# Kernel optimization log

Hardware: AMD Instinct MI355X
Metric: run time of the kernel (lower is better)

The kernel has to match this reference:

```python
import jax, jax.numpy as jnp
import numpy as np


def setup_inputs() -> dict:
    key = jax.random.key(0)
    k1, k2, k3 = jax.random.split(key, 3)
    B, N = 1024, 4096
    kp3d = jax.random.normal(k1, (B, N, 3), dtype=jnp.float32)
    ref_points = jax.random.uniform(k2, (B, N, 2), dtype=jnp.float32)
    weight = jax.random.uniform(k3, (B, N), dtype=jnp.float32)
    return {"kp3d": kp3d, "ref_points": ref_points, "weight": weight}


def reference(kp3d, ref_points, weight):
    # Projected 2D coords (perspective output already applied upstream).
    x = (kp3d[:, :, 0] + 1.0) * 0.5          # [B, N]
    y = 1.0 - (kp3d[:, :, 1] + 1.0) * 0.5    # [B, N]
    z = kp3d[:, :, 2]                         # [B, N]

    # my_normalize: per-batch-row min-max normalization (vectorized).
    # NOTE: result is computed but unused by the loss, exactly as in the
    # original forward (z = my_normalize(z) is dead afterwards).
    z_min = jnp.min(z, axis=1, keepdims=True)
    z_max = jnp.max(z, axis=1, keepdims=True)
    z_norm = (z - z_min) / (z_max - z_min)    # [B, N]

    kp2d = jnp.stack((x, y), axis=2)          # [B, N, 2]

    # kp_loss: weighted per-point 2D Euclidean distance, summed.
    diff = kp2d - ref_points                  # [B, N, 2]
    dist = jnp.sqrt(jnp.sum(diff * diff, axis=2))  # [B, N]
    loss = jnp.sum(weight * dist)
    # z_norm is dead code in the original; loss is the sole output.
    return loss
```

## Files before the change

### kernel.cpp

```cpp
#include <hip/hip_runtime.h>


__global__ void zero_out_kernel(float* out) {
    out[0] = 0.0f;
}

__global__ __launch_bounds__(256) void viewpoint_loss_kernel(
    const float* __restrict__ kp3d,
    const float* __restrict__ ref,
    const float* __restrict__ w,
    float* __restrict__ out,
    int ngroups)
{
    const float4* kp4 = (const float4*)kp3d;
    const float4* rf4 = (const float4*)ref;
    const float4* w4  = (const float4*)w;

    float acc = 0.0f;
    int stride = gridDim.x * blockDim.x;
    for (int g = blockIdx.x * blockDim.x + threadIdx.x; g < ngroups; g += stride) {
        float4 k0 = kp4[3 * g + 0];
        float4 k1 = kp4[3 * g + 1];
        float4 k2 = kp4[3 * g + 2];
        float4 r0 = rf4[2 * g + 0];
        float4 r1 = rf4[2 * g + 1];
        float4 wv = w4[g];

        float dx, dy;

        dx = fmaf(k0.x, 0.5f, 0.5f) - r0.x;
        dy = fmaf(k0.y, -0.5f, 0.5f) - r0.y;
        acc += wv.x * sqrtf(fmaf(dx, dx, dy * dy));

        dx = fmaf(k0.w, 0.5f, 0.5f) - r0.z;
        dy = fmaf(k1.x, -0.5f, 0.5f) - r0.w;
        acc += wv.y * sqrtf(fmaf(dx, dx, dy * dy));

        dx = fmaf(k1.z, 0.5f, 0.5f) - r1.x;
        dy = fmaf(k1.w, -0.5f, 0.5f) - r1.y;
        acc += wv.z * sqrtf(fmaf(dx, dx, dy * dy));

        dx = fmaf(k2.y, 0.5f, 0.5f) - r1.z;
        dy = fmaf(k2.z, -0.5f, 0.5f) - r1.w;
        acc += wv.w * sqrtf(fmaf(dx, dx, dy * dy));
    }

    #pragma unroll
    for (int off = 32; off > 0; off >>= 1)
        acc += __shfl_down(acc, off, 64);

    __shared__ float wave_sums[4];
    int lane = threadIdx.x & 63;
    int wid  = threadIdx.x >> 6;
    if (lane == 0) wave_sums[wid] = acc;
    __syncthreads();

    if (threadIdx.x == 0) {
        float s = wave_sums[0] + wave_sums[1] + wave_sums[2] + wave_sums[3];
        atomicAdd(out, s);
    }
}

extern "C" void kernel_launch(void* const* d_in, const int* in_sizes, int n_in,
                              void* d_out, int out_size, void* d_ws, size_t ws_size,
                              hipStream_t stream) {
    const float* kp3d = (const float*)d_in[0];
    const float* ref  = (const float*)d_in[1];
    const float* w    = (const float*)d_in[2];
    float* out = (float*)d_out;

    int npts = in_sizes[2];
    int ngroups = npts / 4;

    zero_out_kernel<<<1, 1, 0, stream>>>(out);

    viewpoint_loss_kernel<<<1024, 256, 0, stream>>>(kp3d, ref, w, out, ngroups);
}
```

Before: 120.0 us.

## Replace grid-stride atomic reduction with unrolled two-pass partial-sum reduction

```diff
diff --git a/kernel.cpp b/kernel.cpp
--- a/kernel.cpp
+++ b/kernel.cpp
@@ -1,49 +1,93 @@
 #include <hip/hip_runtime.h>
 
 
-__global__ void zero_out_kernel(float* out) {
-    out[0] = 0.0f;
-}
+#define TPB 256
 
-__global__ __launch_bounds__(256) void viewpoint_loss_kernel(
+__global__ __launch_bounds__(TPB) void viewpoint_partial_kernel(
     const float* __restrict__ kp3d,
     const float* __restrict__ ref,
     const float* __restrict__ w,
-    float* __restrict__ out,
-    int ngroups)
+    float* __restrict__ partials,
+    int T)
 {
     const float4* kp4 = (const float4*)kp3d;
     const float4* rf4 = (const float4*)ref;
     const float4* w4  = (const float4*)w;
 
+    int tid = blockIdx.x * TPB + threadIdx.x;
+    int g0 = tid;
+    int g1 = tid + T;
+
+    float4 a0 = kp4[3 * g0 + 0];
+    float4 a1 = kp4[3 * g0 + 1];
+    float4 a2 = kp4[3 * g0 + 2];
+    float4 b0 = kp4[3 * g1 + 0];
+    float4 b1 = kp4[3 * g1 + 1];
+    float4 b2 = kp4[3 * g1 + 2];
+    float4 r00 = rf4[2 * g0 + 0];
+    float4 r01 = rf4[2 * g0 + 1];
+    float4 r10 = rf4[2 * g1 + 0];
+    float4 r11 = rf4[2 * g1 + 1];
+    float4 w0 = w4[g0];
+    float4 w1 = w4[g1];
+
     float acc = 0.0f;
-    int stride = gridDim.x * blockDim.x;
-    for (int g = blockIdx.x * blockDim.x + threadIdx.x; g < ngroups; g += stride) {
-        float4 k0 = kp4[3 * g + 0];
-        float4 k1 = kp4[3 * g + 1];
-        float4 k2 = kp4[3 * g + 2];
-        float4 r0 = rf4[2 * g + 0];
-        float4 r1 = rf4[2 * g + 1];
-        float4 wv = w4[g];
+    float dx, dy;
 
-        float dx, dy;
+    dx = fmaf(a0.x, 0.5f, 0.5f) - r00.x;
+    dy = fmaf(a0.y, -0.5f, 0.5f) - r00.y;
+    acc += w0.x * sqrtf(fmaf(dx, dx, dy * dy));
 
-        dx = fmaf(k0.x, 0.5f, 0.5f) - r0.x;
-        dy = fmaf(k0.y, -0.5f, 0.5f) - r0.y;
-        acc += wv.x * sqrtf(fmaf(dx, dx, dy * dy));
+    dx = fmaf(a0.w, 0.5f, 0.5f) - r00.z;
+    dy = fmaf(a1.x, -0.5f, 0.5f) - r00.w;
+    acc += w0.y * sqrtf(fmaf(dx, dx, dy * dy));
 
-        dx = fmaf(k0.w, 0.5f, 0.5f) - r0.z;
-        dy = fmaf(k1.x, -0.5f, 0.5f) - r0.w;
-        acc += wv.y * sqrtf(fmaf(dx, dx, dy * dy));
+    dx = fmaf(a1.z, 0.5f, 0.5f) - r01.x;
+    dy = fmaf(a1.w, -0.5f, 0.5f) - r01.y;
+    acc += w0.z * sqrtf(fmaf(dx, dx, dy * dy));
 
-        dx = fmaf(k1.z, 0.5f, 0.5f) - r1.x;
-        dy = fmaf(k1.w, -0.5f, 0.5f) - r1.y;
-        acc += wv.z * sqrtf(fmaf(dx, dx, dy * dy));
+    dx = fmaf(a2.y, 0.5f, 0.5f) - r01.z;
+    dy = fmaf(a2.z, -0.5f, 0.5f) - r01.w;
+    acc += w0.w * sqrtf(fmaf(dx, dx, dy * dy));
 
-        dx = fmaf(k2.y, 0.5f, 0.5f) - r1.z;
-        dy = fmaf(k2.z, -0.5f, 0.5f) - r1.w;
-        acc += wv.w * sqrtf(fmaf(dx, dx, dy * dy));
+    dx = fmaf(b0.x, 0.5f, 0.5f) - r10.x;
+    dy = fmaf(b0.y, -0.5f, 0.5f) - r10.y;
+    acc += w1.x * sqrtf(fmaf(dx, dx, dy * dy));
+
+    dx = fmaf(b0.w, 0.5f, 0.5f) - r10.z;
+    dy = fmaf(b1.x, -0.5f, 0.5f) - r10.w;
+    acc += w1.y * sqrtf(fmaf(dx, dx, dy * dy));
+
+    dx = fmaf(b1.z, 0.5f, 0.5f) - r11.x;
+    dy = fmaf(b1.w, -0.5f, 0.5f) - r11.y;
+    acc += w1.z * sqrtf(fmaf(dx, dx, dy * dy));
+
+    dx = fmaf(b2.y, 0.5f, 0.5f) - r11.z;
+    dy = fmaf(b2.z, -0.5f, 0.5f) - r11.w;
+    acc += w1.w * sqrtf(fmaf(dx, dx, dy * dy));
+
+    #pragma unroll
+    for (int off = 32; off > 0; off >>= 1)
+        acc += __shfl_down(acc, off, 64);
+
+    __shared__ float wave_sums[TPB / 64];
+    int lane = threadIdx.x & 63;
+    int wid  = threadIdx.x >> 6;
+    if (lane == 0) wave_sums[wid] = acc;
+    __syncthreads();
+
+    if (threadIdx.x == 0) {
+        partials[blockIdx.x] = wave_sums[0] + wave_sums[1]
+                             + wave_sums[2] + wave_sums[3];
     }
+}
+
+__global__ __launch_bounds__(256) void final_reduce_kernel(
+    const float* __restrict__ partials, float* __restrict__ out, int n)
+{
+    float acc = 0.0f;
+    for (int i = threadIdx.x; i < n; i += 256)
+        acc += partials[i];
 
     #pragma unroll
     for (int off = 32; off > 0; off >>= 1)
@@ -55,10 +99,8 @@
     if (lane == 0) wave_sums[wid] = acc;
     __syncthreads();
 
-    if (threadIdx.x == 0) {
-        float s = wave_sums[0] + wave_sums[1] + wave_sums[2] + wave_sums[3];
-        atomicAdd(out, s);
-    }
+    if (threadIdx.x == 0)
+        out[0] = wave_sums[0] + wave_sums[1] + wave_sums[2] + wave_sums[3];
 }
 
 extern "C" void kernel_launch(void* const* d_in, const int* in_sizes, int n_in,
@@ -68,11 +110,13 @@
     const float* ref  = (const float*)d_in[1];
     const float* w    = (const float*)d_in[2];
     float* out = (float*)d_out;
+    float* partials = (float*)d_ws;
 
     int npts = in_sizes[2];
     int ngroups = npts / 4;
+    int T = ngroups / 2;
+    int blocks = T / TPB;
 
-    zero_out_kernel<<<1, 1, 0, stream>>>(out);
-
-    viewpoint_loss_kernel<<<1024, 256, 0, stream>>>(kp3d, ref, w, out, ngroups);
+    viewpoint_partial_kernel<<<blocks, TPB, 0, stream>>>(kp3d, ref, w, partials, T);
+    final_reduce_kernel<<<1, 256, 0, stream>>>(partials, out, blocks);
 }
```

After: 117.9 us. No clear change (-1.7%).
